# Optimization experiments

Hardware: AMD Instinct MI355X
Metric: run time of the kernel (lower is better)

Reference implementation:

```python
import jax, jax.numpy as jnp
import numpy as np

RRELU_SLOPE = (1.0 / 8.0 + 1.0 / 3.0) / 2.0  # F.rrelu eval mode
N_ENT, N_REL2, H, E, B, T = 20000, 460, 128, 400000, 1024, 8


def _lin(x, W, b):
    return x @ W.T + b  # torch nn.Linear convention


def _gru_cell(x, h, w_ih, w_hh, b_ih, b_hh):
    gi = x @ w_ih.T + b_ih
    gh = h @ w_hh.T + b_hh
    i_r, i_z, i_n = jnp.split(gi, 3, axis=1)
    h_r, h_z, h_n = jnp.split(gh, 3, axis=1)
    r = jax.nn.sigmoid(i_r + h_r)
    z = jax.nn.sigmoid(i_z + h_z)
    n = jnp.tanh(i_n + r * h_n)
    return (1.0 - z) * n + z * h


def setup_inputs() -> dict:
    key = jax.random.key(0)
    ks = jax.random.split(key, 24)
    s = 0.02
    inp = {
        'ent_emb': jax.random.normal(ks[0], (N_ENT, H), jnp.float32),
        'rel_emb': jax.random.normal(ks[1], (N_REL2, H), jnp.float32),
        'weight_neighbor': jax.random.normal(ks[2], (H, H), jnp.float32) * s,
        'loop_weight': jax.random.normal(ks[3], (H, H), jnp.float32) * s,
        'evolve_loop_weight': jax.random.normal(ks[4], (H, H), jnp.float32) * s,
        'w_ih': jax.random.normal(ks[5], (3 * H, H), jnp.float32) * s,
        'w_hh': jax.random.normal(ks[6], (3 * H, H), jnp.float32) * s,
        'b_ih': jnp.zeros((3 * H,), jnp.float32),
        'b_hh': jnp.zeros((3 * H,), jnp.float32),
        'W_map1': jax.random.normal(ks[7], (2 * H, H), jnp.float32) * s,
        'b_map1': jnp.zeros((2 * H,), jnp.float32),
        'W_map2': jax.random.normal(ks[8], (H, 2 * H), jnp.float32) * s,
        'b_map2': jnp.zeros((H,), jnp.float32),
        'W_h1': jax.random.normal(ks[9], (H, H), jnp.float32) * s,
        'b_h1': jnp.zeros((H,), jnp.float32),
        'W_h2': jax.random.normal(ks[10], (H, H), jnp.float32) * s,
        'b_h2': jnp.zeros((H,), jnp.float32),
        'W_align': jax.random.normal(ks[11], (H, H), jnp.float32) * s,
        'b_align': jnp.zeros((H,), jnp.float32),
        'W_attn': jax.random.normal(ks[12], (H, H), jnp.float32) * s,
        'b_attn': jnp.zeros((H,), jnp.float32),
    }
    u = jax.random.uniform(ks[13], (B, T * N_REL2), jnp.float32)
    mask = jax.random.uniform(ks[14], (B, T * N_REL2)) > 0.7  # sparse history
    inp['partial_embeding'] = u * mask
    inp['edge_src'] = jax.random.randint(ks[15], (E,), 0, N_ENT, jnp.int32)
    inp['edge_dst'] = jax.random.randint(ks[16], (E,), 0, N_ENT, jnp.int32)
    inp['edge_type'] = jax.random.randint(ks[17], (E,), 0, N_REL2, jnp.int32)
    sub = jax.random.randint(ks[18], (B,), 0, N_ENT, jnp.int32)
    rel = jax.random.randint(ks[19], (B,), 0, N_REL2, jnp.int32)
    obj = jax.random.randint(ks[20], (B,), 0, N_ENT, jnp.int32)
    inp['triples'] = jnp.stack([sub, rel, obj], axis=1)
    return inp


def reference(ent_emb, rel_emb, weight_neighbor, loop_weight, evolve_loop_weight,
              w_ih, w_hh, b_ih, b_hh, W_map1, b_map1, W_map2, b_map2,
              W_h1, b_h1, W_h2, b_h2, W_align, b_align, W_attn, b_attn,
              partial_embeding, edge_src, edge_dst, edge_type, triples):
    # ---- UnionRGCNLayer: gather-transform-scatter ----
    h = ent_emb
    msg = (h[edge_src] + rel_emb[edge_type]) @ weight_neighbor          # [E, H]
    agg = jax.ops.segment_sum(msg, edge_dst, num_segments=N_ENT)        # [N, H]
    deg = jax.ops.segment_sum(jnp.ones((edge_dst.shape[0],), h.dtype), edge_dst,
                              num_segments=N_ENT)
    norm = jnp.where(deg > 0, 1.0 / jnp.where(deg > 0, deg, 1.0), 0.0)[:, None]
    loop = jnp.where((deg > 0)[:, None], h @ loop_weight, h @ evolve_loop_weight)
    x = agg * norm + loop
    pre_emb = jnp.where(x >= 0, x, x * RRELU_SLOPE)                     # rrelu (eval)

    # ---- PathPredictor.forward_back ----
    mapped_rel = _lin(_lin(rel_emb, W_map1, b_map1), W_map2, b_map2)    # [2R, H]
    q_rel = mapped_rel[triples[:, 1]]                                   # [B, H]
    A = _lin(q_rel, W_attn, b_attn) @ mapped_rel.T                      # [B, 2R]
    hist = partial_embeding.reshape(B, T, N_REL2).transpose(1, 0, 2)    # [T, B, 2R]

    def step(gh, cur):
        attn = cur * A
        attn = jax.nn.softmax(jnp.where(attn == 0, -1e9, attn), axis=1)
        rel_path = attn @ mapped_rel                                    # [B, H]
        return _gru_cell(rel_path, gh, w_ih, w_hh, b_ih, b_hh), None

    gru_hidden, _ = jax.lax.scan(step, jnp.zeros((B, H), pre_emb.dtype), hist)
    predicted_hist = 0.1 * _lin(_lin(q_rel, W_h1, b_h1), W_h2, b_h2) + q_rel
    match_loss = jnp.mean((predicted_hist - gru_hidden) ** 2)

    # ---- forward_forth, distmult scoring ----
    gh2 = _gru_cell(q_rel, predicted_hist, w_ih, w_hh, b_ih, b_hh)      # [B, H]
    sub_emb = pre_emb[triples[:, 0]]
    aligned_all = _lin(pre_emb, W_align, b_align)                       # [N, H]
    score_ = (_lin(sub_emb, W_align, b_align) * gh2) @ aligned_all.T    # [B, N]
    score = jax.nn.sigmoid(score_)
    # BCE(score, one_hot(obj)) without materializing labels:
    logp = jax.nn.log_sigmoid(score_)
    log1mp = jax.nn.log_sigmoid(-score_)
    total = -jnp.sum(log1mp)
    rows = jnp.arange(B)
    total = total + jnp.sum(log1mp[rows, triples[:, 2]] - logp[rows, triples[:, 2]])
    path_loss = total / (B * N_ENT)
    return score, match_loss, path_loss
```

## Files before the change

kernel.cpp:

```cpp
#include <hip/hip_runtime.h>

typedef unsigned short u16;
typedef unsigned int u32;
typedef __attribute__((ext_vector_type(8))) short bf8v;
typedef __attribute__((ext_vector_type(4))) float f4v;

#define RRELU_SLOPE 0.22916666667f

__device__ inline float bf2f(u16 u){ unsigned int i = ((unsigned int)u) << 16; float f; __builtin_memcpy(&f, &i, 4); return f; }
__device__ inline u16 f2bf(float f){ unsigned int i; __builtin_memcpy(&i, &f, 4); unsigned int r = (i + 0x7fffu + ((i >> 16) & 1u)) >> 16; return (u16)r; }
__device__ inline float frcp(float x){ return __builtin_amdgcn_rcpf(x); }
__device__ inline float fsigm(float x){ return frcp(1.f + __expf(-x)); }
__device__ inline float ftanh(float x){ return 2.f * frcp(1.f + __expf(-2.f * x)) - 1.f; }

__global__ __launch_bounds__(256) void prep_k(
    const float* __restrict__ Wn, const float* __restrict__ Wl, const float* __restrict__ We,
    const float* __restrict__ wih, const float* __restrict__ whh,
    const float* __restrict__ m1, const float* __restrict__ m2,
    const float* __restrict__ h1, const float* __restrict__ h2,
    const float* __restrict__ attn, const float* __restrict__ alg, const float* __restrict__ rel,
    const float* __restrict__ ent, const float* __restrict__ bat, const float* __restrict__ bh1,
    u16* __restrict__ Bcat, u16* __restrict__ wihb, u16* __restrict__ whhb,
    u16* __restrict__ m1b, u16* __restrict__ m2b, u16* __restrict__ h1b, u16* __restrict__ h2b,
    u16* __restrict__ attnb, u16* __restrict__ algb, u16* __restrict__ relb,
    u16* __restrict__ entb, float* __restrict__ bias2)
{
    int id = blockIdx.x * 256 + threadIdx.x;
    if (id < 49152) {
        int n = id / 384, k = id % 384;
        float v = (k < 128) ? Wn[k*128 + n] : (k < 256 ? Wl[(k-128)*128 + n] : We[(k-256)*128 + n]);
        Bcat[id] = f2bf(v); return;
    }
    id -= 49152;
    if (id < 49152) { wihb[id] = f2bf(wih[id]); return; } id -= 49152;
    if (id < 49152) { whhb[id] = f2bf(whh[id]); return; } id -= 49152;
    if (id < 32768) { m1b[id]  = f2bf(m1[id]);  return; } id -= 32768;
    if (id < 32768) { m2b[id]  = f2bf(m2[id]);  return; } id -= 32768;
    if (id < 16384) { h1b[id]  = f2bf(h1[id]);  return; } id -= 16384;
    if (id < 16384) { h2b[id]  = f2bf(h2[id]);  return; } id -= 16384;
    if (id < 16384) { attnb[id]= f2bf(attn[id]);return; } id -= 16384;
    if (id < 16384) { algb[id] = f2bf(alg[id]); return; } id -= 16384;
    if (id < 58880) { relb[id] = f2bf(rel[id]); return; } id -= 58880;
    if (id < 2560000) { entb[id] = f2bf(ent[id]); return; } id -= 2560000;
    if (id < 256) { bias2[id] = (id < 128) ? bat[id] : bh1[id - 128]; }
}

__global__ __launch_bounds__(256) void hist_k(
    const int* __restrict__ dst, int* __restrict__ hist, int E)
{
    int e = blockIdx.x * 256 + threadIdx.x;
    if (e < E) atomicAdd(&hist[dst[e]], 1);
}

__global__ __launch_bounds__(1024) void scan_k(
    const int* __restrict__ hist, int* __restrict__ starts, int* __restrict__ cursor)
{
    __shared__ int part[1024];
    int t = threadIdx.x;
    int base = t * 20;
    int s = 0;
    for (int j = 0; j < 20; ++j) { int idx = base + j; if (idx < 20000) s += hist[idx]; }
    part[t] = s;
    __syncthreads();
    for (int off = 1; off < 1024; off <<= 1) {
        int v = (t >= off) ? part[t - off] : 0;
        __syncthreads();
        part[t] += v;
        __syncthreads();
    }
    int run = (t > 0) ? part[t - 1] : 0;
    for (int j = 0; j < 20; ++j) {
        int idx = base + j;
        if (idx < 20000) { starts[idx] = run; cursor[idx] = run; run += hist[idx]; }
    }
    if (t == 1023) starts[20000] = run;
}

__global__ __launch_bounds__(256) void scatter_k(
    const int* __restrict__ src, const int* __restrict__ dst, const int* __restrict__ typ,
    int* __restrict__ cursor, int2* __restrict__ spack, int E)
{
    int e = blockIdx.x * 256 + threadIdx.x;
    if (e >= E) return;
    int d = dst[e];
    int p = atomicAdd(&cursor[d], 1);
    spack[p] = make_int2(src[e], typ[e]);
}

__global__ __launch_bounds__(64) void agg_acat_k(
    const int2* __restrict__ spack, const int* __restrict__ starts,
    const u32* __restrict__ hb, const u32* __restrict__ rb, u32* __restrict__ Acat32)
{
    int i = blockIdx.x;
    int lane = threadIdx.x;
    int s0 = starts[i], s1 = starts[i + 1];
    float sx = 0.f, sy = 0.f;
    for (int e = s0; e < s1; ++e) {
        int2 st = spack[e];
        u32 a = hb[(long)st.x * 64 + lane];
        u32 r = rb[(long)st.y * 64 + lane];
        sx += bf2f((u16)(a & 0xffff)) + bf2f((u16)(r & 0xffff));
        sy += bf2f((u16)(a >> 16))    + bf2f((u16)(r >> 16));
    }
    bool has = s1 > s0;
    float nrm = has ? frcp((float)(s1 - s0)) : 0.f;
    u32 hv = hb[(long)i * 64 + lane];
    u32 agg = (u32)f2bf(sx * nrm) | ((u32)f2bf(sy * nrm) << 16);
    long o = (long)i * 192 + lane;
    Acat32[o]       = agg;
    Acat32[o + 64]  = has ? hv : 0u;
    Acat32[o + 128] = has ? 0u : hv;
}

__global__ __launch_bounds__(256) void gemm_nt(
    const u16* __restrict__ A, const u16* __restrict__ B, const float* __restrict__ bias,
    float* __restrict__ Cf, u16* __restrict__ Cbf, u16* __restrict__ CT,
    const u16* __restrict__ residb, const int* __restrict__ arows,
    int M, int N, int K, int lda, int ldb, int ldc, int ldct, int arow_stride,
    float rscale, int epi)
{
    int tid = threadIdx.x;
    int wave = tid >> 6, lane = tid & 63;
    int ln = lane & 15, q = lane >> 4;
    int bm = blockIdx.y * 64 + wave * 16;
    int bn = blockIdx.x * 64;
    int am = bm + ln; if (am >= M) am = M - 1;
    long ar = arows ? (long)arows[(long)am * arow_stride] : (long)am;
    const u16* Ap = A + ar * lda;
    int br[4];
#pragma unroll
    for (int nt = 0; nt < 4; ++nt) { int n = bn + nt*16 + ln; br[nt] = (n < N) ? n : (N - 1); }
    f4v acc[4] = {};
    for (int kc = 0; kc < K; kc += 32) {
        bf8v af = *(const bf8v*)(Ap + kc + q*8);
#pragma unroll
        for (int nt = 0; nt < 4; ++nt) {
            bf8v bv = *(const bf8v*)(B + (long)br[nt]*ldb + kc + q*8);
            acc[nt] = __builtin_amdgcn_mfma_f32_16x16x32_bf16(af, bv, acc[nt], 0, 0, 0);
        }
    }
#pragma unroll
    for (int nt = 0; nt < 4; ++nt) {
        int n = bn + nt*16 + ln;
        if (n >= N) continue;
        float bv = bias ? bias[n] : 0.f;
#pragma unroll
        for (int r = 0; r < 4; ++r) {
            int m = bm + q*4 + r;
            if (m >= M) continue;
            float v = acc[nt][r] + bv;
            if (epi == 1) v = (v >= 0.f) ? v : v * RRELU_SLOPE;
            if (residb)  v = rscale * v + bf2f(residb[(long)m*ldc + n]);
            long ci = (long)m*ldc + n;
            if (Cf)  Cf[ci]  = v;
            if (Cbf) Cbf[ci] = f2bf(v);
            if (CT)  CT[(long)n*ldct + m] = f2bf(v);
        }
    }
}

__global__ __launch_bounds__(256) void qrel_k(
    const u16* __restrict__ mapb, const int* __restrict__ trip,
    u16* __restrict__ qrelb, u16* __restrict__ X)
{
    int id = blockIdx.x * 256 + threadIdx.x;
    int b = id >> 7, k = id & 127;
    int r = trip[b*3 + 1];
    u16 v = mapb[r*128 + k];
    qrelb[id] = v;
    X[(long)(8192 + b)*128 + k] = v;
}

__global__ __launch_bounds__(64) void softmax_k(
    const float* __restrict__ Amat, const float* __restrict__ part, u16* __restrict__ Xattn)
{
    int row = blockIdx.x;
    int t = row >> 10, b = row & 1023;
    int lane = threadIdx.x;
    const float* arow = Amat + (long)b*460;
    const float* crow = part + (long)b*3680 + t*460;
    float v[8], e[8];
    float m = -1e30f;
#pragma unroll
    for (int i = 0; i < 8; ++i) {
        int r = i*64 + lane;
        e[i] = 0.f;
        if (r < 460) {
            float x = crow[r] * arow[r];
            x = (x == 0.f) ? -1e9f : x;
            v[i] = x; m = fmaxf(m, x);
        } else v[i] = -1e30f;
    }
#pragma unroll
    for (int off = 32; off; off >>= 1) m = fmaxf(m, __shfl_xor(m, off));
    float sum = 0.f;
#pragma unroll
    for (int i = 0; i < 8; ++i) {
        int r = i*64 + lane;
        if (r < 460) { e[i] = __expf(v[i] - m); sum += e[i]; }
    }
#pragma unroll
    for (int off = 32; off; off >>= 1) sum += __shfl_xor(sum, off);
    float inv = frcp(sum);
#pragma unroll
    for (int i = 0; i < 8; ++i) {
        int r = i*64 + lane;
        if (r < 460)      Xattn[(long)row*480 + r] = f2bf(e[i] * inv);
        else if (r < 480) Xattn[(long)row*480 + r] = 0;
    }
}

__global__ __launch_bounds__(256) void gru_k(
    const float* __restrict__ gi, const u16* __restrict__ whhb, const float* __restrict__ bhh,
    const float* __restrict__ pred, float* __restrict__ gh2, float* __restrict__ match_acc)
{
    __shared__ u16  hbf[16][136];
    __shared__ float hf [4][128];
    __shared__ float ghl[4][388];
    __shared__ float red[4];
    int tid = threadIdx.x;
    int wave = tid >> 6, lane = tid & 63;
    int ln = lane & 15, q = lane >> 4;
    int bb = blockIdx.x * 4;
    for (int i = tid; i < 16*136; i += 256) hbf[i/136][i%136] = 0;
    for (int i = tid; i < 4*128; i += 256) hf[i>>7][i&127] = 0.f;
    bf8v bfrag[6][4];
#pragma unroll
    for (int nt = 0; nt < 6; ++nt)
#pragma unroll
        for (int kc = 0; kc < 4; ++kc)
            bfrag[nt][kc] = *(const bf8v*)(whhb + (long)(wave*96 + nt*16 + ln)*128 + kc*32 + q*8);
    int k = tid & 127;
    float br = bhh[k], bz = bhh[128 + k], bn_ = bhh[256 + k];
    __syncthreads();
    float msum = 0.f;
    for (int t = 0; t <= 8; ++t) {
        float gr[2], gz[2], gn[2], pv[2];
        long girow0 = (t < 8) ? ((long)t*1024 + bb) : (8192 + bb);
#pragma unroll
        for (int it = 0; it < 2; ++it) {
            int m = it*2 + (tid >> 7);
            const float* gp = gi + (girow0 + m)*384;
            gr[it] = gp[k]; gz[it] = gp[128 + k]; gn[it] = gp[256 + k];
            pv[it] = (t >= 7) ? pred[(long)(bb + m)*128 + k] : 0.f;
        }
        if (t == 8) {
#pragma unroll
            for (int it = 0; it < 2; ++it) {
                int m = it*2 + (tid >> 7);
                hf[m][k] = pv[it]; hbf[m][k] = f2bf(pv[it]);
            }
            __syncthreads();
        }
        f4v acc[6] = {};
#pragma unroll
        for (int kc = 0; kc < 4; ++kc) {
            bf8v af = *(const bf8v*)&hbf[ln][kc*32 + q*8];
#pragma unroll
            for (int nt = 0; nt < 6; ++nt)
                acc[nt] = __builtin_amdgcn_mfma_f32_16x16x32_bf16(af, bfrag[nt][kc], acc[nt], 0, 0, 0);
        }
        if (q == 0) {
#pragma unroll
            for (int nt = 0; nt < 6; ++nt)
#pragma unroll
                for (int r = 0; r < 4; ++r)
                    ghl[r][wave*96 + nt*16 + ln] = acc[nt][r];
        }
        __syncthreads();
#pragma unroll
        for (int it = 0; it < 2; ++it) {
            int m = it*2 + (tid >> 7);
            float rr = fsigm(gr[it] + ghl[m][k] + br);
            float zz = fsigm(gz[it] + ghl[m][128 + k] + bz);
            float nn = ftanh(gn[it] + rr * (ghl[m][256 + k] + bn_));
            float hn = (1.f - zz) * nn + zz * hf[m][k];
            if (t == 7) { float d = pv[it] - hn; msum += d*d; }
            if (t == 8) { gh2[(long)(bb + m)*128 + k] = hn; }
            else        { hf[m][k] = hn; hbf[m][k] = f2bf(hn); }
        }
        __syncthreads();
    }
#pragma unroll
    for (int off = 32; off; off >>= 1) msum += __shfl_down(msum, off);
    if (lane == 0) red[wave] = msum;
    __syncthreads();
    if (tid == 0) atomicAdd(match_acc, red[0] + red[1] + red[2] + red[3]);
}

__global__ __launch_bounds__(128) void vo_k(
    const float* __restrict__ subl, const float* __restrict__ gh2,
    const u16* __restrict__ AL, const int* __restrict__ trip,
    u16* __restrict__ V, float* __restrict__ obj_acc)
{
    int b = blockIdx.x, k = threadIdx.x;
    u16 vb = f2bf(subl[b*128 + k] * gh2[b*128 + k]);
    V[b*128 + k] = vb;
    int obj = trip[b*3 + 2];
    float s = bf2f(vb) * bf2f(AL[(long)obj*128 + k]);
#pragma unroll
    for (int off = 32; off; off >>= 1) s += __shfl_down(s, off);
    __shared__ float red2[2];
    if ((k & 63) == 0) red2[k >> 6] = s;
    __syncthreads();
    if (k == 0) atomicAdd(obj_acc, -(red2[0] + red2[1]));
}

__global__ __launch_bounds__(512) void score_k(
    const u16* __restrict__ V, const u16* __restrict__ AL,
    float* __restrict__ out, float* __restrict__ sp_acc, int N)
{
    __shared__ float stage[8][2048];
    int tid = threadIdx.x;
    int wave = tid >> 6, lane = tid & 63;
    int ln = lane & 15, q = lane >> 4;
    int bm = blockIdx.y * 128 + (wave >> 2) * 64;
    int bn = blockIdx.x * 128 + (wave & 3) * 32;
    bool valid = bn < N;
    int br[2];
#pragma unroll
    for (int nt = 0; nt < 2; ++nt) { int n = bn + nt*16 + ln; br[nt] = (n < N) ? n : (N - 1); }
    f4v acc[4][2] = {};
    for (int kc = 0; kc < 128; kc += 32) {
        bf8v a[4], b[2];
#pragma unroll
        for (int mt = 0; mt < 4; ++mt)
            a[mt] = *(const bf8v*)(V + (long)(bm + mt*16 + ln)*128 + kc + q*8);
#pragma unroll
        for (int nt = 0; nt < 2; ++nt)
            b[nt] = *(const bf8v*)(AL + (long)br[nt]*128 + kc + q*8);
#pragma unroll
        for (int mt = 0; mt < 4; ++mt)
#pragma unroll
            for (int nt = 0; nt < 2; ++nt)
                acc[mt][nt] = __builtin_amdgcn_mfma_f32_16x16x32_bf16(a[mt], b[nt], acc[mt][nt], 0, 0, 0);
    }
    float lsum = 0.f;
    float* st = stage[wave];
#pragma unroll
    for (int mt = 0; mt < 4; ++mt)
#pragma unroll
    for (int nt = 0; nt < 2; ++nt)
#pragma unroll
    for (int r = 0; r < 4; ++r) {
        float s = acc[mt][nt][r];
        float e = __expf(-fabsf(s));
        float d = 1.f + e;
        float inv = frcp(d);
        st[(mt*16 + q*4 + r)*32 + nt*16 + ln] = (s >= 0.f) ? inv : e * inv;
        lsum += fmaxf(s, 0.f) + __logf(d);
    }
    if (!valid) lsum = 0.f;
    if (valid) {
        int row0 = lane >> 3, c4 = (lane & 7) << 2;
#pragma unroll
        for (int i = 0; i < 8; ++i) {
            int row = i*8 + row0;
            f4v vv = *(const f4v*)&st[row*32 + c4];
            __builtin_nontemporal_store(vv, (f4v*)&out[(long)(bm + row)*N + bn + c4]);
        }
    }
#pragma unroll
    for (int off = 32; off; off >>= 1) lsum += __shfl_xor(lsum, off);
    __shared__ float red[8];
    if (lane == 0) red[wave] = lsum;
    __syncthreads();
    if (tid == 0) {
        float tsum = 0.f;
#pragma unroll
        for (int w = 0; w < 8; ++w) tsum += red[w];
        atomicAdd(sp_acc, tsum);
    }
}

__global__ void final_k(const float* __restrict__ acc, float* __restrict__ out)
{
    out[20480000] = acc[0] / (1024.f * 128.f);
    out[20480001] = (acc[1] + acc[2]) / (1024.f * 20000.f);
}

extern "C" void kernel_launch(void* const* d_in, const int* in_sizes, int n_in,
                              void* d_out, int out_size, void* d_ws, size_t ws_size,
                              hipStream_t stream)
{
    const float* ent  = (const float*)d_in[0];
    const float* rel  = (const float*)d_in[1];
    const float* Wn   = (const float*)d_in[2];
    const float* Wl   = (const float*)d_in[3];
    const float* We   = (const float*)d_in[4];
    const float* wih  = (const float*)d_in[5];
    const float* whh  = (const float*)d_in[6];
    const float* b_ih = (const float*)d_in[7];
    const float* b_hh = (const float*)d_in[8];
    const float* Wm1  = (const float*)d_in[9];
    const float* bm1  = (const float*)d_in[10];
    const float* Wm2  = (const float*)d_in[11];
    const float* bm2  = (const float*)d_in[12];
    const float* Wh1  = (const float*)d_in[13];
    const float* bh1  = (const float*)d_in[14];
    const float* Wh2  = (const float*)d_in[15];
    const float* bh2  = (const float*)d_in[16];
    const float* Wal  = (const float*)d_in[17];
    const float* bal  = (const float*)d_in[18];
    const float* Wat  = (const float*)d_in[19];
    const float* bat  = (const float*)d_in[20];
    const float* part = (const float*)d_in[21];
    const int* esrc   = (const int*)d_in[22];
    const int* edst   = (const int*)d_in[23];
    const int* etyp   = (const int*)d_in[24];
    const int* trip   = (const int*)d_in[25];
    float* out = (float*)d_out;
    const int E = in_sizes[22];

    char* ws = (char*)d_ws;
    size_t off = 0;
    auto alloc = [&](size_t bytes) { size_t o = off; off = (off + bytes + 255) & ~(size_t)255; return o; };

    size_t o_acc   = alloc(256);
    size_t o_hist  = alloc(20000 * 4);
    size_t o_mapT  = alloc(128 * 480 * 2);
    size_t zend = off;
    size_t o_starts= alloc(20004 * 4);
    size_t o_cur   = alloc(20000 * 4);
    size_t o_spack = alloc((size_t)E * 8);
    size_t o_entb  = alloc((size_t)20000 * 128 * 2);
    size_t o_acat  = alloc((size_t)20000 * 384 * 2);
    size_t o_pre   = alloc((size_t)20000 * 128 * 2);
    size_t o_aln   = alloc((size_t)20000 * 128 * 2);
    size_t o_bcat  = alloc(128 * 384 * 2);
    size_t o_wih   = alloc(384 * 128 * 2);
    size_t o_whh   = alloc(384 * 128 * 2);
    size_t o_m1    = alloc(256 * 128 * 2);
    size_t o_m2    = alloc(128 * 256 * 2);
    size_t o_ath   = alloc(2 * 128 * 128 * 2);
    size_t o_h2    = alloc(128 * 128 * 2);
    size_t o_al    = alloc(128 * 128 * 2);
    size_t o_rel   = alloc(460 * 128 * 2);
    size_t o_t1    = alloc(460 * 256 * 2);
    size_t o_map   = alloc(460 * 128 * 2);
    size_t o_qrel  = alloc(1024 * 128 * 2);
    size_t o_qt    = alloc((size_t)1024 * 256 * 2);
    size_t o_b2    = alloc(256 * 4);
    size_t o_pred  = alloc(1024 * 128 * 4);
    size_t o_amat  = alloc((size_t)1024 * 460 * 4);
    size_t o_xat   = alloc((size_t)8192 * 480 * 2);
    size_t o_X     = alloc((size_t)9216 * 128 * 2);
    size_t o_gi    = alloc((size_t)9216 * 384 * 4);
    size_t o_subl  = alloc(1024 * 128 * 4);
    size_t o_gh2   = alloc(1024 * 128 * 4);
    size_t o_V     = alloc(1024 * 128 * 2);

    float* accp  = (float*)(ws + o_acc);
    int* histp   = (int*)(ws + o_hist);
    u16* mapT    = (u16*)(ws + o_mapT);
    int* startsp = (int*)(ws + o_starts);
    int* curp    = (int*)(ws + o_cur);
    int2* spack  = (int2*)(ws + o_spack);
    u16* entb    = (u16*)(ws + o_entb);
    u16* acat    = (u16*)(ws + o_acat);
    u16* preb    = (u16*)(ws + o_pre);
    u16* alnb    = (u16*)(ws + o_aln);
    u16* bcat    = (u16*)(ws + o_bcat);
    u16* wihb    = (u16*)(ws + o_wih);
    u16* whhb    = (u16*)(ws + o_whh);
    u16* m1b     = (u16*)(ws + o_m1);
    u16* m2b     = (u16*)(ws + o_m2);
    u16* atb     = (u16*)(ws + o_ath);
    u16* h1b     = atb + 128 * 128;
    u16* h2b     = (u16*)(ws + o_h2);
    u16* alb     = (u16*)(ws + o_al);
    u16* relb    = (u16*)(ws + o_rel);
    u16* t1b     = (u16*)(ws + o_t1);
    u16* mapb    = (u16*)(ws + o_map);
    u16* qrelb   = (u16*)(ws + o_qrel);
    u16* qtb     = (u16*)(ws + o_qt);
    float* bias2 = (float*)(ws + o_b2);
    float* predf = (float*)(ws + o_pred);
    float* amat  = (float*)(ws + o_amat);
    u16* xat     = (u16*)(ws + o_xat);
    u16* Xb      = (u16*)(ws + o_X);
    float* gif   = (float*)(ws + o_gi);
    float* subl  = (float*)(ws + o_subl);
    float* gh2f  = (float*)(ws + o_gh2);
    u16* Vb      = (u16*)(ws + o_V);

    hipMemsetAsync(ws, 0, zend, stream);

    prep_k<<<11319, 256, 0, stream>>>(Wn, Wl, We, wih, whh, Wm1, Wm2, Wh1, Wh2, Wat, Wal, rel,
                                      ent, bat, bh1,
                                      bcat, wihb, whhb, m1b, m2b, h1b, h2b, atb, alb, relb,
                                      entb, bias2);

    int eb = (E + 255) / 256;
    hist_k<<<eb, 256, 0, stream>>>(edst, histp, E);
    scan_k<<<1, 1024, 0, stream>>>(histp, startsp, curp);
    scatter_k<<<eb, 256, 0, stream>>>(esrc, edst, etyp, curp, spack, E);
    agg_acat_k<<<20000, 64, 0, stream>>>(spack, startsp, (const u32*)entb, (const u32*)relb, (u32*)acat);

    gemm_nt<<<dim3(2, 313), 256, 0, stream>>>(acat, bcat, nullptr, nullptr, preb, nullptr, nullptr, nullptr,
                                              20000, 128, 384, 384, 384, 128, 0, 0, 0.f, 1);
    gemm_nt<<<dim3(2, 313), 256, 0, stream>>>(preb, alb, bal, nullptr, alnb, nullptr, nullptr, nullptr,
                                              20000, 128, 128, 128, 128, 128, 0, 0, 0.f, 0);
    gemm_nt<<<dim3(4, 8), 256, 0, stream>>>(relb, m1b, bm1, nullptr, t1b, nullptr, nullptr, nullptr,
                                            460, 256, 128, 128, 128, 256, 0, 0, 0.f, 0);
    gemm_nt<<<dim3(2, 8), 256, 0, stream>>>(t1b, m2b, bm2, nullptr, mapb, mapT, nullptr, nullptr,
                                            460, 128, 256, 256, 256, 128, 480, 0, 0.f, 0);

    qrel_k<<<512, 256, 0, stream>>>(mapb, trip, qrelb, Xb);

    gemm_nt<<<dim3(4, 16), 256, 0, stream>>>(qrelb, atb, bias2, nullptr, qtb, nullptr, nullptr, nullptr,
                                             1024, 256, 128, 128, 128, 256, 0, 0, 0.f, 0);
    gemm_nt<<<dim3(2, 16), 256, 0, stream>>>(qtb + 128, h2b, bh2, predf, nullptr, nullptr, qrelb, nullptr,
                                             1024, 128, 128, 256, 128, 128, 0, 0, 0.1f, 0);
    gemm_nt<<<dim3(8, 16), 256, 0, stream>>>(qtb, mapb, nullptr, amat, nullptr, nullptr, nullptr, nullptr,
                                             1024, 460, 128, 256, 128, 460, 0, 0, 0.f, 0);

    softmax_k<<<8192, 64, 0, stream>>>(amat, part, xat);

    gemm_nt<<<dim3(2, 128), 256, 0, stream>>>(xat, mapT, nullptr, nullptr, Xb, nullptr, nullptr, nullptr,
                                              8192, 128, 480, 480, 480, 128, 0, 0, 0.f, 0);
    gemm_nt<<<dim3(6, 144), 256, 0, stream>>>(Xb, wihb, b_ih, gif, nullptr, nullptr, nullptr, nullptr,
                                              9216, 384, 128, 128, 128, 384, 0, 0, 0.f, 0);
    gemm_nt<<<dim3(2, 16), 256, 0, stream>>>(preb, alb, bal, subl, nullptr, nullptr, nullptr, trip,
                                             1024, 128, 128, 128, 128, 128, 0, 3, 0.f, 0);

    gru_k<<<256, 256, 0, stream>>>(gif, whhb, b_hh, predf, gh2f, accp + 0);

    vo_k<<<1024, 128, 0, stream>>>(subl, gh2f, alnb, trip, Vb, accp + 2);

    score_k<<<dim3(157, 8), 512, 0, stream>>>(Vb, alnb, out, accp + 1, 20000);

    final_k<<<1, 1, 0, stream>>>(accp, out);

    (void)in_sizes; (void)n_in; (void)out_size; (void)ws_size;
}
```

Before: 470.4 us.

## Fuse rel-map MLP, query projections, and softmax with attention GEMM; unroll aggregation

Merges the two chained GEMMs for the relation mapping MLP into one kernel that keeps the intermediate in shared memory. It also fuses the query-attention and history-prediction GEMMs, and fuses the per-row softmax with the attention-times-mapped-relation GEMM so the bf16 attention matrix never goes to global memory. Separately, the edge aggregation loop is unrolled by four so more gathers are in flight. Several launches and intermediate buffers go away, but the fused kernels run on very few blocks (8 and 16), which limits parallelism.

```diff
diff --git a/kernel.cpp b/kernel.cpp
--- a/kernel.cpp
+++ b/kernel.cpp
@@ -95,7 +95,23 @@
     int lane = threadIdx.x;
     int s0 = starts[i], s1 = starts[i + 1];
     float sx = 0.f, sy = 0.f;
-    for (int e = s0; e < s1; ++e) {
+    int e = s0;
+    for (; e + 4 <= s1; e += 4) {
+        int2 st0 = spack[e], st1 = spack[e+1], st2 = spack[e+2], st3 = spack[e+3];
+        u32 a0 = hb[(long)st0.x * 64 + lane]; u32 r0 = rb[(long)st0.y * 64 + lane];
+        u32 a1 = hb[(long)st1.x * 64 + lane]; u32 r1 = rb[(long)st1.y * 64 + lane];
+        u32 a2 = hb[(long)st2.x * 64 + lane]; u32 r2 = rb[(long)st2.y * 64 + lane];
+        u32 a3 = hb[(long)st3.x * 64 + lane]; u32 r3 = rb[(long)st3.y * 64 + lane];
+        sx += bf2f((u16)(a0 & 0xffff)) + bf2f((u16)(r0 & 0xffff));
+        sy += bf2f((u16)(a0 >> 16))    + bf2f((u16)(r0 >> 16));
+        sx += bf2f((u16)(a1 & 0xffff)) + bf2f((u16)(r1 & 0xffff));
+        sy += bf2f((u16)(a1 >> 16))    + bf2f((u16)(r1 >> 16));
+        sx += bf2f((u16)(a2 & 0xffff)) + bf2f((u16)(r2 & 0xffff));
+        sy += bf2f((u16)(a2 >> 16))    + bf2f((u16)(r2 >> 16));
+        sx += bf2f((u16)(a3 & 0xffff)) + bf2f((u16)(r3 & 0xffff));
+        sy += bf2f((u16)(a3 >> 16))    + bf2f((u16)(r3 >> 16));
+    }
+    for (; e < s1; ++e) {
         int2 st = spack[e];
         u32 a = hb[(long)st.x * 64 + lane];
         u32 r = rb[(long)st.y * 64 + lane];
@@ -159,6 +175,60 @@
     }
 }
 
+__global__ __launch_bounds__(256) void fuse_map_k(
+    const u16* __restrict__ relb, const u16* __restrict__ m1b, const float* __restrict__ bm1,
+    const u16* __restrict__ m2b, const float* __restrict__ bm2,
+    u16* __restrict__ mapb, u16* __restrict__ mapT)
+{
+    __shared__ u16 t1l[4][16][264];
+    int tid = threadIdx.x;
+    int wave = tid >> 6, lane = tid & 63;
+    int ln = lane & 15, q = lane >> 4;
+    int base = blockIdx.x * 64 + wave * 16;
+    int arow = base + ln; if (arow > 459) arow = 459;
+    const u16* Ap = relb + arow * 128;
+    f4v acc1[16] = {};
+    for (int kc = 0; kc < 128; kc += 32) {
+        bf8v af = *(const bf8v*)(Ap + kc + q*8);
+#pragma unroll
+        for (int nt = 0; nt < 16; ++nt) {
+            bf8v bv = *(const bf8v*)(m1b + (nt*16 + ln)*128 + kc + q*8);
+            acc1[nt] = __builtin_amdgcn_mfma_f32_16x16x32_bf16(af, bv, acc1[nt], 0, 0, 0);
+        }
+    }
+#pragma unroll
+    for (int nt = 0; nt < 16; ++nt) {
+        int n = nt*16 + ln;
+        float bv = bm1[n];
+#pragma unroll
+        for (int r = 0; r < 4; ++r)
+            t1l[wave][q*4 + r][n] = f2bf(acc1[nt][r] + bv);
+    }
+    f4v acc2[8] = {};
+    for (int kc = 0; kc < 256; kc += 32) {
+        bf8v af = *(const bf8v*)&t1l[wave][ln][kc + q*8];
+#pragma unroll
+        for (int nt = 0; nt < 8; ++nt) {
+            bf8v bv = *(const bf8v*)(m2b + (nt*16 + ln)*256 + kc + q*8);
+            acc2[nt] = __builtin_amdgcn_mfma_f32_16x16x32_bf16(af, bv, acc2[nt], 0, 0, 0);
+        }
+    }
+#pragma unroll
+    for (int nt = 0; nt < 8; ++nt) {
+        int n = nt*16 + ln;
+        float bv = bm2[n];
+#pragma unroll
+        for (int r = 0; r < 4; ++r) {
+            int m = base + q*4 + r;
+            if (m < 460) {
+                u16 hv = f2bf(acc2[nt][r] + bv);
+                mapb[m*128 + n] = hv;
+                mapT[n*480 + m] = hv;
+            }
+        }
+    }
+}
+
 __global__ __launch_bounds__(256) void qrel_k(
     const u16* __restrict__ mapb, const int* __restrict__ trip,
     u16* __restrict__ qrelb, u16* __restrict__ X)
@@ -171,42 +241,129 @@
     X[(long)(8192 + b)*128 + k] = v;
 }
 
-__global__ __launch_bounds__(64) void softmax_k(
-    const float* __restrict__ Amat, const float* __restrict__ part, u16* __restrict__ Xattn)
-{
-    int row = blockIdx.x;
-    int t = row >> 10, b = row & 1023;
-    int lane = threadIdx.x;
-    const float* arow = Amat + (long)b*460;
-    const float* crow = part + (long)b*3680 + t*460;
-    float v[8], e[8];
-    float m = -1e30f;
-#pragma unroll
-    for (int i = 0; i < 8; ++i) {
-        int r = i*64 + lane;
-        e[i] = 0.f;
-        if (r < 460) {
-            float x = crow[r] * arow[r];
-            x = (x == 0.f) ? -1e9f : x;
-            v[i] = x; m = fmaxf(m, x);
-        } else v[i] = -1e30f;
-    }
-#pragma unroll
-    for (int off = 32; off; off >>= 1) m = fmaxf(m, __shfl_xor(m, off));
-    float sum = 0.f;
-#pragma unroll
-    for (int i = 0; i < 8; ++i) {
-        int r = i*64 + lane;
-        if (r < 460) { e[i] = __expf(v[i] - m); sum += e[i]; }
-    }
-#pragma unroll
-    for (int off = 32; off; off >>= 1) sum += __shfl_xor(sum, off);
-    float inv = frcp(sum);
-#pragma unroll
-    for (int i = 0; i < 8; ++i) {
-        int r = i*64 + lane;
-        if (r < 460)      Xattn[(long)row*480 + r] = f2bf(e[i] * inv);
-        else if (r < 480) Xattn[(long)row*480 + r] = 0;
+__global__ __launch_bounds__(256) void fuse_qt_k(
+    const u16* __restrict__ qrelb, const u16* __restrict__ atb, const float* __restrict__ bias2,
+    const u16* __restrict__ h2b, const float* __restrict__ bh2,
+    u16* __restrict__ atq, float* __restrict__ pred)
+{
+    __shared__ u16 th1l[4][16][136];
+    int tid = threadIdx.x;
+    int wave = tid >> 6, lane = tid & 63;
+    int ln = lane & 15, q = lane >> 4;
+    int base = blockIdx.x * 64 + wave * 16;
+    const u16* Ap = qrelb + (base + ln) * 128;
+    f4v acc1[16] = {};
+    for (int kc = 0; kc < 128; kc += 32) {
+        bf8v af = *(const bf8v*)(Ap + kc + q*8);
+#pragma unroll
+        for (int nt = 0; nt < 16; ++nt) {
+            bf8v bv = *(const bf8v*)(atb + (nt*16 + ln)*128 + kc + q*8);
+            acc1[nt] = __builtin_amdgcn_mfma_f32_16x16x32_bf16(af, bv, acc1[nt], 0, 0, 0);
+        }
+    }
+#pragma unroll
+    for (int nt = 0; nt < 16; ++nt) {
+        int n = nt*16 + ln;
+        float bv = bias2[n];
+#pragma unroll
+        for (int r = 0; r < 4; ++r) {
+            float x = acc1[nt][r] + bv;
+            if (nt < 8) atq[(base + q*4 + r)*128 + n] = f2bf(x);
+            else        th1l[wave][q*4 + r][n - 128] = f2bf(x);
+        }
+    }
+    f4v acc2[8] = {};
+    for (int kc = 0; kc < 128; kc += 32) {
+        bf8v af = *(const bf8v*)&th1l[wave][ln][kc + q*8];
+#pragma unroll
+        for (int nt = 0; nt < 8; ++nt) {
+            bf8v bv = *(const bf8v*)(h2b + (nt*16 + ln)*128 + kc + q*8);
+            acc2[nt] = __builtin_amdgcn_mfma_f32_16x16x32_bf16(af, bv, acc2[nt], 0, 0, 0);
+        }
+    }
+#pragma unroll
+    for (int nt = 0; nt < 8; ++nt) {
+        int n = nt*16 + ln;
+        float bv = bh2[n];
+#pragma unroll
+        for (int r = 0; r < 4; ++r) {
+            int m = base + q*4 + r;
+            pred[(long)m*128 + n] = 0.1f * (acc2[nt][r] + bv) + bf2f(qrelb[(long)m*128 + n]);
+        }
+    }
+}
+
+__global__ __launch_bounds__(256) void smrp_k(
+    const float* __restrict__ Amat, const float* __restrict__ part,
+    const u16* __restrict__ mapT, u16* __restrict__ X)
+{
+    __shared__ u16 xls[32][488];
+    int tid = threadIdx.x;
+    int wave = tid >> 6, lane = tid & 63;
+    int base = blockIdx.x * 32;
+    int t = base >> 10, b0 = base & 1023;
+    for (int j = 0; j < 8; ++j) {
+        int rl = wave*8 + j;
+        int b = b0 + rl;
+        const float* arow = Amat + (long)b*460;
+        const float* crow = part + (long)b*3680 + t*460;
+        float v[8], e[8];
+        float m = -1e30f;
+#pragma unroll
+        for (int i = 0; i < 8; ++i) {
+            int r = i*64 + lane;
+            if (r < 460) {
+                float x = crow[r] * arow[r];
+                x = (x == 0.f) ? -1e9f : x;
+                v[i] = x; m = fmaxf(m, x);
+            } else v[i] = -1e30f;
+        }
+#pragma unroll
+        for (int off = 32; off; off >>= 1) m = fmaxf(m, __shfl_xor(m, off));
+        float sum = 0.f;
+#pragma unroll
+        for (int i = 0; i < 8; ++i) {
+            int r = i*64 + lane;
+            e[i] = 0.f;
+            if (r < 460) { e[i] = __expf(v[i] - m); sum += e[i]; }
+        }
+#pragma unroll
+        for (int off = 32; off; off >>= 1) sum += __shfl_xor(sum, off);
+        float inv = frcp(sum);
+#pragma unroll
+        for (int i = 0; i < 8; ++i) {
+            int r = i*64 + lane;
+            if (r < 460)      xls[rl][r] = f2bf(e[i] * inv);
+            else if (r < 488) xls[rl][r] = 0;
+        }
+    }
+    __syncthreads();
+    int ln = lane & 15, q = lane >> 4;
+    f4v acc[2][2] = {};
+    for (int kc = 0; kc < 480; kc += 32) {
+        bf8v a[2], bfr[2];
+#pragma unroll
+        for (int mt = 0; mt < 2; ++mt)
+            a[mt] = *(const bf8v*)&xls[mt*16 + ln][kc + q*8];
+#pragma unroll
+        for (int nt = 0; nt < 2; ++nt)
+            bfr[nt] = *(const bf8v*)(mapT + (wave*32 + nt*16 + ln)*480 + kc + q*8);
+#pragma unroll
+        for (int mt = 0; mt < 2; ++mt)
+#pragma unroll
+            for (int nt = 0; nt < 2; ++nt)
+                acc[mt][nt] = __builtin_amdgcn_mfma_f32_16x16x32_bf16(a[mt], bfr[nt], acc[mt][nt], 0, 0, 0);
+    }
+#pragma unroll
+    for (int mt = 0; mt < 2; ++mt)
+#pragma unroll
+    for (int nt = 0; nt < 2; ++nt) {
+        int n = wave*32 + nt*16 + ln;
+#pragma unroll
+        for (int r = 0; r < 4; ++r) {
+            int m = base + mt*16 + q*4 + r;
+            X[(long)m*128 + n] = f2bf(acc[mt][nt][r]);
+        }
     }
 }
 
@@ -436,14 +593,12 @@
     size_t o_h2    = alloc(128 * 128 * 2);
     size_t o_al    = alloc(128 * 128 * 2);
     size_t o_rel   = alloc(460 * 128 * 2);
-    size_t o_t1    = alloc(460 * 256 * 2);
     size_t o_map   = alloc(460 * 128 * 2);
     size_t o_qrel  = alloc(1024 * 128 * 2);
-    size_t o_qt    = alloc((size_t)1024 * 256 * 2);
+    size_t o_atq   = alloc(1024 * 128 * 2);
     size_t o_b2    = alloc(256 * 4);
     size_t o_pred  = alloc(1024 * 128 * 4);
     size_t o_amat  = alloc((size_t)1024 * 460 * 4);
-    size_t o_xat   = alloc((size_t)8192 * 480 * 2);
     size_t o_X     = alloc((size_t)9216 * 128 * 2);
     size_t o_gi    = alloc((size_t)9216 * 384 * 4);
     size_t o_subl  = alloc(1024 * 128 * 4);
@@ -470,14 +625,12 @@
     u16* h2b     = (u16*)(ws + o_h2);
     u16* alb     = (u16*)(ws + o_al);
     u16* relb    = (u16*)(ws + o_rel);
-    u16* t1b     = (u16*)(ws + o_t1);
     u16* mapb    = (u16*)(ws + o_map);
     u16* qrelb   = (u16*)(ws + o_qrel);
-    u16* qtb     = (u16*)(ws + o_qt);
+    u16* atqb    = (u16*)(ws + o_atq);
     float* bias2 = (float*)(ws + o_b2);
     float* predf = (float*)(ws + o_pred);
     float* amat  = (float*)(ws + o_amat);
-    u16* xat     = (u16*)(ws + o_xat);
     u16* Xb      = (u16*)(ws + o_X);
     float* gif   = (float*)(ws + o_gi);
     float* subl  = (float*)(ws + o_subl);
@@ -501,24 +654,18 @@
                                               20000, 128, 384, 384, 384, 128, 0, 0, 0.f, 1);
     gemm_nt<<<dim3(2, 313), 256, 0, stream>>>(preb, alb, bal, nullptr, alnb, nullptr, nullptr, nullptr,
                                               20000, 128, 128, 128, 128, 128, 0, 0, 0.f, 0);
-    gemm_nt<<<dim3(4, 8), 256, 0, stream>>>(relb, m1b, bm1, nullptr, t1b, nullptr, nullptr, nullptr,
-                                            460, 256, 128, 128, 128, 256, 0, 0, 0.f, 0);
-    gemm_nt<<<dim3(2, 8), 256, 0, stream>>>(t1b, m2b, bm2, nullptr, mapb, mapT, nullptr, nullptr,
-                                            460, 128, 256, 256, 256, 128, 480, 0, 0.f, 0);
+
+    fuse_map_k<<<8, 256, 0, stream>>>(relb, m1b, bm1, m2b, bm2, mapb, mapT);
 
     qrel_k<<<512, 256, 0, stream>>>(mapb, trip, qrelb, Xb);
 
-    gemm_nt<<<dim3(4, 16), 256, 0, stream>>>(qrelb, atb, bias2, nullptr, qtb, nullptr, nullptr, nullptr,
-                                             1024, 256, 128, 128, 128, 256, 0, 0, 0.f, 0);
-    gemm_nt<<<dim3(2, 16), 256, 0, stream>>>(qtb + 128, h2b, bh2, predf, nullptr, nullptr, qrelb, nullptr,
-                                             1024, 128, 128, 256, 128, 128, 0, 0, 0.1f, 0);
-    gemm_nt<<<dim3(8, 16), 256, 0, stream>>>(qtb, mapb, nullptr, amat, nullptr, nullptr, nullptr, nullptr,
-                                             1024, 460, 128, 256, 128, 460, 0, 0, 0.f, 0);
-
-    softmax_k<<<8192, 64, 0, stream>>>(amat, part, xat);
-
-    gemm_nt<<<dim3(2, 128), 256, 0, stream>>>(xat, mapT, nullptr, nullptr, Xb, nullptr, nullptr, nullptr,
-                                              8192, 128, 480, 480, 480, 128, 0, 0, 0.f, 0);
+    fuse_qt_k<<<16, 256, 0, stream>>>(qrelb, atb, bias2, h2b, bh2, atqb, predf);
+
+    gemm_nt<<<dim3(8, 16), 256, 0, stream>>>(atqb, mapb, nullptr, amat, nullptr, nullptr, nullptr, nullptr,
+                                             1024, 460, 128, 128, 128, 460, 0, 0, 0.f, 0);
+
+    smrp_k<<<256, 256, 0, stream>>>(amat, part, mapT, Xb);
+
     gemm_nt<<<dim3(6, 144), 256, 0, stream>>>(Xb, wihb, b_ih, gif, nullptr, nullptr, nullptr, nullptr,
                                               9216, 384, 128, 128, 128, 384, 0, 0, 0.f, 0);
     gemm_nt<<<dim3(2, 16), 256, 0, stream>>>(preb, alb, bal, subl, nullptr, nullptr, nullptr, trip,
```

Measured after the change: 470.1 us. About the same (-0.1%).
